# Performance work log

Hardware: AMD Instinct MI355X
Metric: run time of the kernel (lower is better)

Reference implementation:

```python
import jax, jax.numpy as jnp
import numpy as np

N = 100000
IN_F, HID, OUT = 256, 128, 64
NNZ = 1600000
EQ = 200000


def setup_inputs() -> dict:
    key = jax.random.key(0)
    ks = jax.random.split(key, 10)
    x = jax.random.normal(ks[0], (N, IN_F), dtype=jnp.float32)
    adj_rows = jnp.sort(jax.random.randint(ks[1], (NNZ,), 0, N, dtype=jnp.int32))
    adj_cols = jax.random.randint(ks[2], (NNZ,), 0, N, dtype=jnp.int32)
    adj_vals = jax.random.uniform(ks[3], (NNZ,), dtype=jnp.float32)
    edge_index = jax.random.randint(ks[4], (2, EQ), 0, N, dtype=jnp.int32)
    # params (torch Linear default init: U(-1/sqrt(fan_in), 1/sqrt(fan_in)))
    s1 = 1.0 / np.sqrt(IN_F)
    W1 = jax.random.uniform(ks[5], (IN_F, HID), minval=-s1, maxval=s1, dtype=jnp.float32)
    b1 = jax.random.uniform(ks[6], (HID,), minval=-s1, maxval=s1, dtype=jnp.float32)
    s2 = 1.0 / np.sqrt(HID)
    W2 = jax.random.uniform(ks[7], (HID, OUT), minval=-s2, maxval=s2, dtype=jnp.float32)
    b2 = jax.random.uniform(ks[8], (OUT,), minval=-s2, maxval=s2, dtype=jnp.float32)
    return {"x": x, "adj_rows": adj_rows, "adj_cols": adj_cols, "adj_vals": adj_vals,
            "edge_index": edge_index, "W1": W1, "b1": b1, "W2": W2, "b2": b2}


def spmm(rows, cols, vals, dense):
    # out[i,:] = sum_{e: rows[e]==i} vals[e] * dense[cols[e],:]
    msgs = vals[:, None] * dense[cols]  # [nnz, d]
    return jax.ops.segment_sum(msgs, rows, num_segments=N)


def reference(x, adj_rows, adj_cols, adj_vals, edge_index, W1, b1, W2, b2):
    # GCN layer 1: linear then sparse aggregation
    h = spmm(adj_rows, adj_cols, adj_vals, x @ W1 + b1)  # [N, HID]
    h = jax.nn.relu(h)  # dropout is identity in eval mode
    # GCN layer 2
    z = spmm(adj_rows, adj_cols, adj_vals, h @ W2 + b2)  # [N, OUT]
    # decode: gather src/dst embeddings, elementwise dot
    src, dst = edge_index[0], edge_index[1]
    return jnp.sum(z[src] * z[dst], axis=1)  # [EQ]
```

## Files before the change

### kernel.cpp

```cpp
#include <hip/hip_runtime.h>

constexpr int NN    = 100000;
constexpr int NNZ_E = 1600000;
constexpr int EQn   = 200000;
constexpr int INF_  = 256;
constexpr int HIDF  = 128;
constexpr int OUTF  = 64;

typedef float  f32x4  __attribute__((ext_vector_type(4)));
typedef short  bf16x8 __attribute__((ext_vector_type(8)));

__device__ inline unsigned short f2bf(float f) {
    union { float f; unsigned int i; } x; x.f = f;
    unsigned int r = x.i + 0x7fffu + ((x.i >> 16) & 1u);
    return (unsigned short)(r >> 16);
}

__device__ inline void gl2lds16(const void* g, void* l) {
    __builtin_amdgcn_global_load_lds(
        (const __attribute__((address_space(1))) void*)g,
        (__attribute__((address_space(3))) void*)l, 16, 0, 0);
}

__global__ __launch_bounds__(256) void prep(const int* __restrict__ rows,
                                            int* __restrict__ ptr,
                                            const float* __restrict__ W1,
                                            const float* __restrict__ W2,
                                            unsigned short* __restrict__ W1t,
                                            unsigned short* __restrict__ W2t) {
    int i = blockIdx.x * 256 + threadIdx.x;
    if (i <= NN) {
        int lo = 0, hi = NNZ_E;
        while (lo < hi) {
            int mid = (lo + hi) >> 1;
            if (rows[mid] < i) lo = mid + 1; else hi = mid;
        }
        ptr[i] = lo;
    }
    if (i < INF_ * HIDF) {
        int k = i >> 7, n = i & 127;
        W1t[n * INF_ + k] = f2bf(W1[i]);
    }
    if (i < HIDF * OUTF) {
        int k = i >> 6, n = i & 63;
        W2t[n * HIDF + k] = f2bf(W2[i]);
    }
}

template<int K, int NCOLS, int TR, int CGB, bool A_IS_BF16>
__global__ __launch_bounds__(512, 1) void gemm_persist(const void* __restrict__ Av,
                                                       const unsigned short* __restrict__ Bt,
                                                       const float* __restrict__ bias,
                                                       unsigned short* __restrict__ C,
                                                       int M) {
    constexpr int KS   = K / 32;
    constexpr int NT   = 2;
    constexpr int CG   = 1 << CGB;
    constexpr int RB   = 8 / CG;
    static_assert(RB * 16 == TR, "tile rows = 16*RB");
    static_assert(CG * 32 == NCOLS, "cols = 32*CG");
    constexpr int ABPR = A_IS_BF16 ? K * 2 : K * 4;
    constexpr int RPC  = 1024 / ABPR;
    constexpr int NCH  = TR / RPC;
    constexpr int CPWW = NCH / 8;
    constexpr int ABUF = NCH * 1040;
    constexpr int PK   = K + 8;
    constexpr int PADW = NCOLS + 8;
    constexpr int BSB  = NCOLS * PK * 2;
    constexpr int EPB  = TR * PADW * 2;
    static_assert(TR * NCOLS / 8 == 512, "one uint4 store per thread");
    __shared__ __align__(16) unsigned char smem[2 * ABUF + BSB + EPB];
    unsigned char*  Ab = smem;
    unsigned short* Bs = (unsigned short*)(smem + 2 * ABUF);
    unsigned short* ep = (unsigned short*)(smem + 2 * ABUF + BSB);

    const int tid  = threadIdx.x;
    const int wave = tid >> 6;
    const int lane = tid & 63;
    const int quad = lane >> 4;
    const int l16  = lane & 15;
    const int cg   = wave & (CG - 1);
    const int rb   = wave >> CGB;

    for (int i = tid; i < NCOLS * K / 8; i += 512) {
        int n = i / (K / 8), kc = (i % (K / 8)) * 8;
        *(uint4*)&Bs[n * PK + kc] = *(const uint4*)&Bt[(size_t)n * K + kc];
    }

    const int ntiles = (M + TR - 1) / TR;
    const char* abase = (const char*)Av;

    auto stage = [&](int b, int tile0) {
        unsigned char* dst = Ab + b * ABUF;
        #pragma unroll
        for (int j = 0; j < CPWW; ++j) {
            int ch = wave * CPWW + j;
            int r0 = tile0 + ch * RPC;
            if (r0 > M - RPC) r0 = M - RPC;
            gl2lds16(abase + (size_t)r0 * ABPR + lane * 16, dst + ch * 1040);
        }
    };

    int t = blockIdx.x, buf = 0;
    if (t < ntiles) stage(0, t * TR);

    for (; t < ntiles; t += gridDim.x) {
        __syncthreads();
        int tn = t + gridDim.x;
        if (tn < ntiles) stage(1 - buf, tn * TR);

        const unsigned char* ab = Ab + buf * ABUF;
        const int arow = rb * 16 + l16;
        f32x4 acc[NT];
        #pragma unroll
        for (int tt = 0; tt < NT; ++tt) acc[tt] = (f32x4){0.f, 0.f, 0.f, 0.f};

        #pragma unroll
        for (int ks = 0; ks < KS; ++ks) {
            bf16x8 af;
            if constexpr (A_IS_BF16) {
                int flat = arow * ABPR + ks * 64 + quad * 16;
                af = *(const bf16x8*)(ab + (flat >> 10) * 1040 + (flat & 1023));
            } else {
                int flat = arow * ABPR + ks * 128 + quad * 32;
                const unsigned char* p = ab + (flat >> 10) * 1040 + (flat & 1023);
                float4 a0 = *(const float4*)p;
                float4 a1 = *(const float4*)(p + 16);
                af[0] = (short)f2bf(a0.x); af[1] = (short)f2bf(a0.y);
                af[2] = (short)f2bf(a0.z); af[3] = (short)f2bf(a0.w);
                af[4] = (short)f2bf(a1.x); af[5] = (short)f2bf(a1.y);
                af[6] = (short)f2bf(a1.z); af[7] = (short)f2bf(a1.w);
            }
            #pragma unroll
            for (int tt = 0; tt < NT; ++tt) {
                bf16x8 bfr = *(const bf16x8*)&Bs[(cg * 32 + tt * 16 + l16) * PK + ks * 32 + quad * 8];
                acc[tt] = __builtin_amdgcn_mfma_f32_16x16x32_bf16(af, bfr, acc[tt], 0, 0, 0);
            }
        }

        #pragma unroll
        for (int tt = 0; tt < NT; ++tt) {
            const int col = cg * 32 + tt * 16 + l16;
            const float bb = bias[col];
            #pragma unroll
            for (int r = 0; r < 4; ++r)
                ep[(rb * 16 + quad * 4 + r) * PADW + col] = f2bf(acc[tt][r] + bb);
        }
        __syncthreads();
        {
            constexpr int CH = NCOLS / 8;
            int r = tid / CH, cc = tid % CH;
            int grow = t * TR + r;
            if (grow < M)
                *(uint4*)&C[(size_t)grow * NCOLS + cc * 8] =
                    *(const uint4*)&ep[r * PADW + cc * 8];
        }
        buf ^= 1;
    }
}

__device__ inline void fma8_bf16(float* acc, uint4 q, float v) {
    union { unsigned int i; float f; } t;
    #pragma unroll
    for (int p = 0; p < 4; ++p) {
        unsigned int w = (&q.x)[p];
        t.i = w << 16;          acc[2*p]   += v * t.f;
        t.i = w & 0xffff0000u;  acc[2*p+1] += v * t.f;
    }
}

template<int D, bool RELU>
__global__ __launch_bounds__(256) void spmm_bf16(const int* __restrict__ ptr,
                                                 const int* __restrict__ cols,
                                                 const float* __restrict__ vals,
                                                 const unsigned short* __restrict__ dense,
                                                 unsigned short* __restrict__ outm) {
    constexpr int LPR = D / 8;
    constexpr int RPB = 256 / LPR;
    const int lane = threadIdx.x % LPR;
    const int row  = blockIdx.x * RPB + threadIdx.x / LPR;
    if (row >= NN) return;

    int e = ptr[row];
    const int e1 = ptr[row + 1];
    const size_t lo8 = (size_t)lane * 8;
    float acc[8] = {};

    if (e < e1) {
        for (; e + 4 <= e1; e += 4) {
            int   c0 = cols[e],   c1 = cols[e+1], c2 = cols[e+2], c3 = cols[e+3];
            float v0 = vals[e],   v1 = vals[e+1], v2 = vals[e+2], v3 = vals[e+3];
            uint4 q0 = *(const uint4*)&dense[(size_t)c0 * D + lo8];
            uint4 q1 = *(const uint4*)&dense[(size_t)c1 * D + lo8];
            uint4 q2 = *(const uint4*)&dense[(size_t)c2 * D + lo8];
            uint4 q3 = *(const uint4*)&dense[(size_t)c3 * D + lo8];
            fma8_bf16(acc, q0, v0);
            fma8_bf16(acc, q1, v1);
            fma8_bf16(acc, q2, v2);
            fma8_bf16(acc, q3, v3);
        }
        if (e < e1) {
            int i1 = e, i2 = e + 1, i3 = e + 2;
            bool k1 = i1 < e1, k2 = i2 < e1, k3 = i3 < e1;
            i1 = k1 ? i1 : e1 - 1; i2 = k2 ? i2 : e1 - 1; i3 = k3 ? i3 : e1 - 1;
            int   c0 = cols[i1],            c1 = cols[i2],            c2 = cols[i3];
            float v0 = k1 ? vals[i1] : 0.f, v1 = k2 ? vals[i2] : 0.f, v2 = k3 ? vals[i3] : 0.f;
            uint4 q0 = *(const uint4*)&dense[(size_t)c0 * D + lo8];
            uint4 q1 = *(const uint4*)&dense[(size_t)c1 * D + lo8];
            uint4 q2 = *(const uint4*)&dense[(size_t)c2 * D + lo8];
            fma8_bf16(acc, q0, v0);
            fma8_bf16(acc, q1, v1);
            fma8_bf16(acc, q2, v2);
        }
    }

    if (RELU) {
        #pragma unroll
        for (int p = 0; p < 8; ++p) acc[p] = fmaxf(acc[p], 0.f);
    }
    uint4 o;
    #pragma unroll
    for (int p = 0; p < 4; ++p)
        (&o.x)[p] = (unsigned int)f2bf(acc[2*p]) | ((unsigned int)f2bf(acc[2*p+1]) << 16);
    *(uint4*)&outm[(size_t)row * D + lo8] = o;
}

__global__ __launch_bounds__(256) void decode_dot_bf16(const unsigned short* __restrict__ z,
                                                       const int* __restrict__ ei,
                                                       float* __restrict__ outv) {
    constexpr int HALF = EQn / 2;
    const int lane = threadIdx.x & 7;
    const int g    = blockIdx.x * 32 + (threadIdx.x >> 3);
    if (g >= HALF) return;
    const int eA = g, eB = g + HALF;
    const int sA = ei[eA],       dA = ei[EQn + eA];
    const int sB = ei[eB],       dB = ei[EQn + eB];
    uint4 qa0 = *(const uint4*)&z[(size_t)sA * 64 + lane * 8];
    uint4 qb0 = *(const uint4*)&z[(size_t)dA * 64 + lane * 8];
    uint4 qa1 = *(const uint4*)&z[(size_t)sB * 64 + lane * 8];
    uint4 qb1 = *(const uint4*)&z[(size_t)dB * 64 + lane * 8];
    union { unsigned int i; float f; } ta, tb;
    float p0 = 0.f, p1 = 0.f;
    #pragma unroll
    for (int k = 0; k < 4; ++k) {
        unsigned int wa = (&qa0.x)[k], wb = (&qb0.x)[k];
        ta.i = wa << 16;         tb.i = wb << 16;         p0 += ta.f * tb.f;
        ta.i = wa & 0xffff0000u; tb.i = wb & 0xffff0000u; p0 += ta.f * tb.f;
        wa = (&qa1.x)[k]; wb = (&qb1.x)[k];
        ta.i = wa << 16;         tb.i = wb << 16;         p1 += ta.f * tb.f;
        ta.i = wa & 0xffff0000u; tb.i = wb & 0xffff0000u; p1 += ta.f * tb.f;
    }
    p0 += __shfl_xor(p0, 1, 8); p1 += __shfl_xor(p1, 1, 8);
    p0 += __shfl_xor(p0, 2, 8); p1 += __shfl_xor(p1, 2, 8);
    p0 += __shfl_xor(p0, 4, 8); p1 += __shfl_xor(p1, 4, 8);
    if (lane == 0) { outv[eA] = p0; outv[eB] = p1; }
}

extern "C" void kernel_launch(void* const* d_in, const int* in_sizes, int n_in,
                              void* d_out, int out_size, void* d_ws, size_t ws_size,
                              hipStream_t stream) {
    (void)in_sizes; (void)n_in; (void)out_size; (void)ws_size;

    const float* x        = (const float*)d_in[0];
    const int*   adj_rows = (const int*)  d_in[1];
    const int*   adj_cols = (const int*)  d_in[2];
    const float* adj_vals = (const float*)d_in[3];
    const int*   ei       = (const int*)  d_in[4];
    const float* W1       = (const float*)d_in[5];
    const float* b1       = (const float*)d_in[6];
    const float* W2       = (const float*)d_in[7];
    const float* b2       = (const float*)d_in[8];
    float* out = (float*)d_out;

    char* ws = (char*)d_ws;
    int* row_ptr = (int*)ws;
    size_t off = ((size_t)(NN + 1) * sizeof(int) + 511) & ~(size_t)511;
    unsigned short* W1t = (unsigned short*)(ws + off);
    unsigned short* W2t = W1t + (size_t)HIDF * INF_;
    unsigned short* slotA = W2t + (size_t)OUTF * HIDF;
    slotA = (unsigned short*)(((size_t)slotA + 511) & ~(size_t)511);
    unsigned short* slotB = slotA + (size_t)NN * HIDF;

    prep<<<(NN + 256) / 256, 256, 0, stream>>>(adj_rows, row_ptr, W1, W2, W1t, W2t);

    gemm_persist<INF_, HIDF, 32, 2, false><<<256, 512, 0, stream>>>(
        x, W1t, b1, slotA, NN);

    spmm_bf16<HIDF, true><<<(NN + 15) / 16, 256, 0, stream>>>(
        row_ptr, adj_cols, adj_vals, slotA, slotB);

    gemm_persist<HIDF, OUTF, 64, 1, true><<<512, 512, 0, stream>>>(
        slotB, W2t, b2, slotA, NN);

    spmm_bf16<OUTF, false><<<(NN + 31) / 32, 256, 0, stream>>>(
        row_ptr, adj_cols, adj_vals, slotA, slotB);

    decode_dot_bf16<<<(EQn / 2) / 32, 256, 0, stream>>>(slotB, ei, out);
}
```

Before: 293.2 us.

## Map one wavefront per SpMM row with 16-edge batched gathers

Both SpMM kernels now assign a whole 64-lane wavefront to each sparse row instead of a few lanes. Each lane handles 2 bf16 columns (D=128) or 1 column (D=64). Column indices and values are loaded as wave-uniform scalars in batches of 16 edges, which raises memory-level parallelism and removes per-lane index loads. In exchange, each gather is narrower (4 or 2 bytes per lane), and rows with about 16 nonzeros leave many predicated tail iterations.

```diff
diff --git a/kernel.cpp b/kernel.cpp
--- a/kernel.cpp
+++ b/kernel.cpp
@@ -159,70 +159,64 @@
     }
 }
 
-__device__ inline void fma8_bf16(float* acc, uint4 q, float v) {
-    union { unsigned int i; float f; } t;
-    #pragma unroll
-    for (int p = 0; p < 4; ++p) {
-        unsigned int w = (&q.x)[p];
-        t.i = w << 16;          acc[2*p]   += v * t.f;
-        t.i = w & 0xffff0000u;  acc[2*p+1] += v * t.f;
-    }
-}
-
 template<int D, bool RELU>
-__global__ __launch_bounds__(256) void spmm_bf16(const int* __restrict__ ptr,
+__global__ __launch_bounds__(256) void spmm_wave(const int* __restrict__ ptr,
                                                  const int* __restrict__ cols,
                                                  const float* __restrict__ vals,
                                                  const unsigned short* __restrict__ dense,
                                                  unsigned short* __restrict__ outm) {
-    constexpr int LPR = D / 8;
-    constexpr int RPB = 256 / LPR;
-    const int lane = threadIdx.x % LPR;
-    const int row  = blockIdx.x * RPB + threadIdx.x / LPR;
+    const int lane = threadIdx.x & 63;
+    int row = __builtin_amdgcn_readfirstlane(blockIdx.x * 4 + (threadIdx.x >> 6));
     if (row >= NN) return;
 
-    int e = ptr[row];
-    const int e1 = ptr[row + 1];
-    const size_t lo8 = (size_t)lane * 8;
-    float acc[8] = {};
-
-    if (e < e1) {
-        for (; e + 4 <= e1; e += 4) {
-            int   c0 = cols[e],   c1 = cols[e+1], c2 = cols[e+2], c3 = cols[e+3];
-            float v0 = vals[e],   v1 = vals[e+1], v2 = vals[e+2], v3 = vals[e+3];
-            uint4 q0 = *(const uint4*)&dense[(size_t)c0 * D + lo8];
-            uint4 q1 = *(const uint4*)&dense[(size_t)c1 * D + lo8];
-            uint4 q2 = *(const uint4*)&dense[(size_t)c2 * D + lo8];
-            uint4 q3 = *(const uint4*)&dense[(size_t)c3 * D + lo8];
-            fma8_bf16(acc, q0, v0);
-            fma8_bf16(acc, q1, v1);
-            fma8_bf16(acc, q2, v2);
-            fma8_bf16(acc, q3, v3);
-        }
-        if (e < e1) {
-            int i1 = e, i2 = e + 1, i3 = e + 2;
-            bool k1 = i1 < e1, k2 = i2 < e1, k3 = i3 < e1;
-            i1 = k1 ? i1 : e1 - 1; i2 = k2 ? i2 : e1 - 1; i3 = k3 ? i3 : e1 - 1;
-            int   c0 = cols[i1],            c1 = cols[i2],            c2 = cols[i3];
-            float v0 = k1 ? vals[i1] : 0.f, v1 = k2 ? vals[i2] : 0.f, v2 = k3 ? vals[i3] : 0.f;
-            uint4 q0 = *(const uint4*)&dense[(size_t)c0 * D + lo8];
-            uint4 q1 = *(const uint4*)&dense[(size_t)c1 * D + lo8];
-            uint4 q2 = *(const uint4*)&dense[(size_t)c2 * D + lo8];
-            fma8_bf16(acc, q0, v0);
-            fma8_bf16(acc, q1, v1);
-            fma8_bf16(acc, q2, v2);
-        }
-    }
-
-    if (RELU) {
-        #pragma unroll
-        for (int p = 0; p < 8; ++p) acc[p] = fmaxf(acc[p], 0.f);
-    }
-    uint4 o;
-    #pragma unroll
-    for (int p = 0; p < 4; ++p)
-        (&o.x)[p] = (unsigned int)f2bf(acc[2*p]) | ((unsigned int)f2bf(acc[2*p+1]) << 16);
-    *(uint4*)&outm[(size_t)row * D + lo8] = o;
+    const int e0 = __builtin_amdgcn_readfirstlane(ptr[row]);
+    const int e1 = __builtin_amdgcn_readfirstlane(ptr[row + 1]);
+
+    float acc0 = 0.f, acc1 = 0.f;
+
+    for (int e = e0; e < e1; e += 16) {
+        int cc[16]; float vv[16];
+        #pragma unroll
+        for (int j = 0; j < 16; ++j) {
+            int idx = e + j;
+            const bool ok = idx < e1;
+            idx = ok ? idx : e1 - 1;
+            cc[j] = cols[idx];
+            vv[j] = ok ? vals[idx] : 0.f;
+        }
+        if constexpr (D == 128) {
+            unsigned int q[16];
+            #pragma unroll
+            for (int j = 0; j < 16; ++j)
+                q[j] = *(const unsigned int*)&dense[(size_t)cc[j] * D + lane * 2];
+            #pragma unroll
+            for (int j = 0; j < 16; ++j) {
+                union { unsigned int i; float f; } t;
+                t.i = q[j] << 16;          acc0 += vv[j] * t.f;
+                t.i = q[j] & 0xffff0000u;  acc1 += vv[j] * t.f;
+            }
+        } else {
+            unsigned int q[16];
+            #pragma unroll
+            for (int j = 0; j < 16; ++j)
+                q[j] = dense[(size_t)cc[j] * D + lane];
+            #pragma unroll
+            for (int j = 0; j < 16; ++j) {
+                union { unsigned int i; float f; } t;
+                t.i = q[j] << 16;
+                acc0 += vv[j] * t.f;
+            }
+        }
+    }
+
+    if (RELU) { acc0 = fmaxf(acc0, 0.f); acc1 = fmaxf(acc1, 0.f); }
+
+    if constexpr (D == 128) {
+        unsigned int o = (unsigned int)f2bf(acc0) | ((unsigned int)f2bf(acc1) << 16);
+        *(unsigned int*)&outm[(size_t)row * D + lane * 2] = o;
+    } else {
+        outm[(size_t)row * D + lane] = f2bf(acc0);
+    }
 }
 
 __global__ __launch_bounds__(256) void decode_dot_bf16(const unsigned short* __restrict__ z,
@@ -286,13 +280,13 @@
     gemm_persist<INF_, HIDF, 32, 2, false><<<256, 512, 0, stream>>>(
         x, W1t, b1, slotA, NN);
 
-    spmm_bf16<HIDF, true><<<(NN + 15) / 16, 256, 0, stream>>>(
+    spmm_wave<HIDF, true><<<(NN + 3) / 4, 256, 0, stream>>>(
         row_ptr, adj_cols, adj_vals, slotA, slotB);
 
     gemm_persist<HIDF, OUTF, 64, 1, true><<<512, 512, 0, stream>>>(
         slotB, W2t, b2, slotA, NN);
 
-    spmm_bf16<OUTF, false><<<(NN + 31) / 32, 256, 0, stream>>>(
+    spmm_wave<OUTF, false><<<(NN + 3) / 4, 256, 0, stream>>>(
         row_ptr, adj_cols, adj_vals, slotA, slotB);
 
     decode_dot_bf16<<<(EQn / 2) / 32, 256, 0, stream>>>(slotB, ei, out);
```

Measured after the change: 351.9 us. 20.0% more time.

## Pack and sort CSR edges per row, use grid-stride SpMM

Applied to the files above, without the earlier changes.

A new kernel packs each row's column index and value into interleaved int2 records. For rows with up to 64 entries it also bitonic-sorts them by column within a wavefront, so gathers from the dense matrix touch addresses in order. Both SpMM launches read the packed records and use a fixed 2048-block grid-stride loop instead of one block per row group. This adds a launch and an extra pass over the edge arrays in exchange for fewer separate index and value loads and possibly better gather locality.

```diff
diff --git a/kernel.cpp b/kernel.cpp
--- a/kernel.cpp
+++ b/kernel.cpp
@@ -44,6 +44,43 @@
     if (i < HIDF * OUTF) {
         int k = i >> 6, n = i & 63;
         W2t[n * HIDF + k] = f2bf(W2[i]);
+    }
+}
+
+__global__ __launch_bounds__(256) void sort_pack(const int* __restrict__ ptr,
+                                                 const int* __restrict__ cols,
+                                                 const float* __restrict__ vals,
+                                                 int2* __restrict__ ep) {
+    const int lane = threadIdx.x & 63;
+    const int row  = blockIdx.x * 4 + (threadIdx.x >> 6);
+    if (row >= NN) return;
+    const int e0 = ptr[row], e1 = ptr[row + 1];
+    const int n  = e1 - e0;
+    if (n <= 0) return;
+    if (n <= 64) {
+        int key; float v;
+        if (lane < n) { key = (cols[e0 + lane] << 6) | lane; v = vals[e0 + lane]; }
+        else          { key = 0x7fffff00 | lane;             v = 0.f; }
+        #pragma unroll
+        for (int k = 2; k <= 64; k <<= 1) {
+            #pragma unroll
+            for (int j = k >> 1; j > 0; j >>= 1) {
+                int   pk_ = __shfl_xor(key, j, 64);
+                float pv_ = __shfl_xor(v,   j, 64);
+                const bool up    = ((lane & k) == 0);
+                const bool lower = ((lane & j) == 0);
+                if ((key > pk_) == (lower == up)) { key = pk_; v = pv_; }
+            }
+        }
+        if (lane < n) {
+            int2 o; o.x = key >> 6; o.y = __float_as_int(v);
+            ep[e0 + lane] = o;
+        }
+    } else {
+        for (int i = lane; i < n; i += 64) {
+            int2 o; o.x = cols[e0 + i]; o.y = __float_as_int(vals[e0 + i]);
+            ep[e0 + i] = o;
+        }
     }
 }
 
@@ -170,59 +207,64 @@
 }
 
 template<int D, bool RELU>
-__global__ __launch_bounds__(256) void spmm_bf16(const int* __restrict__ ptr,
-                                                 const int* __restrict__ cols,
-                                                 const float* __restrict__ vals,
-                                                 const unsigned short* __restrict__ dense,
-                                                 unsigned short* __restrict__ outm) {
+__global__ __launch_bounds__(256) void spmm_sw(const int* __restrict__ ptr,
+                                               const int2* __restrict__ ep,
+                                               const unsigned short* __restrict__ dense,
+                                               unsigned short* __restrict__ outm) {
     constexpr int LPR = D / 8;
     constexpr int RPB = 256 / LPR;
+    constexpr int NRG = (NN + RPB - 1) / RPB;
     const int lane = threadIdx.x % LPR;
-    const int row  = blockIdx.x * RPB + threadIdx.x / LPR;
-    if (row >= NN) return;
-
-    int e = ptr[row];
-    const int e1 = ptr[row + 1];
+    const int rl   = threadIdx.x / LPR;
     const size_t lo8 = (size_t)lane * 8;
-    float acc[8] = {};
-
-    if (e < e1) {
-        for (; e + 4 <= e1; e += 4) {
-            int   c0 = cols[e],   c1 = cols[e+1], c2 = cols[e+2], c3 = cols[e+3];
-            float v0 = vals[e],   v1 = vals[e+1], v2 = vals[e+2], v3 = vals[e+3];
-            uint4 q0 = *(const uint4*)&dense[(size_t)c0 * D + lo8];
-            uint4 q1 = *(const uint4*)&dense[(size_t)c1 * D + lo8];
-            uint4 q2 = *(const uint4*)&dense[(size_t)c2 * D + lo8];
-            uint4 q3 = *(const uint4*)&dense[(size_t)c3 * D + lo8];
-            fma8_bf16(acc, q0, v0);
-            fma8_bf16(acc, q1, v1);
-            fma8_bf16(acc, q2, v2);
-            fma8_bf16(acc, q3, v3);
-        }
+
+    for (int rg = blockIdx.x; rg < NRG; rg += gridDim.x) {
+        const int row = rg * RPB + rl;
+        if (row >= NN) continue;
+
+        int e = ptr[row];
+        const int e1 = ptr[row + 1];
+        float acc[8] = {};
+
         if (e < e1) {
-            int i1 = e, i2 = e + 1, i3 = e + 2;
-            bool k1 = i1 < e1, k2 = i2 < e1, k3 = i3 < e1;
-            i1 = k1 ? i1 : e1 - 1; i2 = k2 ? i2 : e1 - 1; i3 = k3 ? i3 : e1 - 1;
-            int   c0 = cols[i1],            c1 = cols[i2],            c2 = cols[i3];
-            float v0 = k1 ? vals[i1] : 0.f, v1 = k2 ? vals[i2] : 0.f, v2 = k3 ? vals[i3] : 0.f;
-            uint4 q0 = *(const uint4*)&dense[(size_t)c0 * D + lo8];
-            uint4 q1 = *(const uint4*)&dense[(size_t)c1 * D + lo8];
-            uint4 q2 = *(const uint4*)&dense[(size_t)c2 * D + lo8];
-            fma8_bf16(acc, q0, v0);
-            fma8_bf16(acc, q1, v1);
-            fma8_bf16(acc, q2, v2);
-        }
-    }
-
-    if (RELU) {
-        #pragma unroll
-        for (int p = 0; p < 8; ++p) acc[p] = fmaxf(acc[p], 0.f);
-    }
-    uint4 o;
-    #pragma unroll
-    for (int p = 0; p < 4; ++p)
-        (&o.x)[p] = (unsigned int)f2bf(acc[2*p]) | ((unsigned int)f2bf(acc[2*p+1]) << 16);
-    *(uint4*)&outm[(size_t)row * D + lo8] = o;
+            for (; e + 4 <= e1; e += 4) {
+                int2 p0 = ep[e], p1 = ep[e+1], p2 = ep[e+2], p3 = ep[e+3];
+                uint4 q0 = *(const uint4*)&dense[(size_t)p0.x * D + lo8];
+                uint4 q1 = *(const uint4*)&dense[(size_t)p1.x * D + lo8];
+                uint4 q2 = *(const uint4*)&dense[(size_t)p2.x * D + lo8];
+                uint4 q3 = *(const uint4*)&dense[(size_t)p3.x * D + lo8];
+                fma8_bf16(acc, q0, __int_as_float(p0.y));
+                fma8_bf16(acc, q1, __int_as_float(p1.y));
+                fma8_bf16(acc, q2, __int_as_float(p2.y));
+                fma8_bf16(acc, q3, __int_as_float(p3.y));
+            }
+            if (e < e1) {
+                int i1 = e, i2 = e + 1, i3 = e + 2;
+                bool k1 = i1 < e1, k2 = i2 < e1, k3 = i3 < e1;
+                i1 = k1 ? i1 : e1 - 1; i2 = k2 ? i2 : e1 - 1; i3 = k3 ? i3 : e1 - 1;
+                int2 p0 = ep[i1], p1 = ep[i2], p2 = ep[i3];
+                float v0 = k1 ? __int_as_float(p0.y) : 0.f;
+                float v1 = k2 ? __int_as_float(p1.y) : 0.f;
+                float v2 = k3 ? __int_as_float(p2.y) : 0.f;
+                uint4 q0 = *(const uint4*)&dense[(size_t)p0.x * D + lo8];
+                uint4 q1 = *(const uint4*)&dense[(size_t)p1.x * D + lo8];
+                uint4 q2 = *(const uint4*)&dense[(size_t)p2.x * D + lo8];
+                fma8_bf16(acc, q0, v0);
+                fma8_bf16(acc, q1, v1);
+                fma8_bf16(acc, q2, v2);
+            }
+        }
+
+        if (RELU) {
+            #pragma unroll
+            for (int p = 0; p < 8; ++p) acc[p] = fmaxf(acc[p], 0.f);
+        }
+        uint4 o;
+        #pragma unroll
+        for (int p = 0; p < 4; ++p)
+            (&o.x)[p] = (unsigned int)f2bf(acc[2*p]) | ((unsigned int)f2bf(acc[2*p+1]) << 16);
+        *(uint4*)&outm[(size_t)row * D + lo8] = o;
+    }
 }
 
 __global__ __launch_bounds__(256) void decode_dot_bf16(const unsigned short* __restrict__ z,
@@ -280,20 +322,23 @@
     unsigned short* slotA = W2t + (size_t)OUTF * HIDF;
     slotA = (unsigned short*)(((size_t)slotA + 511) & ~(size_t)511);
     unsigned short* slotB = slotA + (size_t)NN * HIDF;
+    int2* epk = (int2*)(((size_t)(slotB + (size_t)NN * HIDF) + 511) & ~(size_t)511);
 
     prep<<<(NN + 256) / 256, 256, 0, stream>>>(adj_rows, row_ptr, W1, W2, W1t, W2t);
+
+    sort_pack<<<(NN + 3) / 4, 256, 0, stream>>>(row_ptr, adj_cols, adj_vals, epk);
 
     gemm_persist<INF_, HIDF, 32, 2, false><<<256, 512, 0, stream>>>(
         x, W1t, b1, slotA, NN);
 
-    spmm_bf16<HIDF, true><<<(NN + 15) / 16, 256, 0, stream>>>(
-        row_ptr, adj_cols, adj_vals, slotA, slotB);
+    spmm_sw<HIDF, true><<<2048, 256, 0, stream>>>(
+        row_ptr, epk, slotA, slotB);
 
     gemm_persist<HIDF, OUTF, 64, 1, true><<<512, 512, 0, stream>>>(
         slotB, W2t, b2, slotA, NN);
 
-    spmm_bf16<OUTF, false><<<(NN + 31) / 32, 256, 0, stream>>>(
-        row_ptr, adj_cols, adj_vals, slotA, slotB);
+    spmm_sw<OUTF, false><<<2048, 256, 0, stream>>>(
+        row_ptr, epk, slotA, slotB);
 
     decode_dot_bf16<<<(EQn / 2) / 32, 256, 0, stream>>>(slotB, ei, out);
 }
```

After: 338.0 us. 15.3% more time.

## Fuse layer-1 SpMM with ReLU and second linear layer via MFMA epilogue

Applied to the files above, without the earlier changes.

The first sparse aggregation kernel now applies ReLU, stages its 16-row bf16 tile in LDS, and multiplies it by W2 (loaded into LDS per block) with MFMA, adding the bias before writing the 64-wide result. This removes the separate second GEMM launch and the global write and read of the 100000x128 hidden matrix. The cost is that every block reloads the 16KB W2 tile and uses more LDS, which may lower occupancy for the latency-bound gather. The shared accumulation loop is factored into a helper, and the workspace buffers are swapped to match.

```diff
diff --git a/kernel.cpp b/kernel.cpp
--- a/kernel.cpp
+++ b/kernel.cpp
@@ -169,6 +169,103 @@
     }
 }
 
+template<int D>
+__device__ inline void spmm_row_accum(int e, int e1,
+                                      const int* __restrict__ cols,
+                                      const float* __restrict__ vals,
+                                      const unsigned short* __restrict__ dense,
+                                      size_t lo8, float* acc) {
+    if (e >= e1) return;
+    for (; e + 4 <= e1; e += 4) {
+        int   c0 = cols[e],   c1 = cols[e+1], c2 = cols[e+2], c3 = cols[e+3];
+        float v0 = vals[e],   v1 = vals[e+1], v2 = vals[e+2], v3 = vals[e+3];
+        uint4 q0 = *(const uint4*)&dense[(size_t)c0 * D + lo8];
+        uint4 q1 = *(const uint4*)&dense[(size_t)c1 * D + lo8];
+        uint4 q2 = *(const uint4*)&dense[(size_t)c2 * D + lo8];
+        uint4 q3 = *(const uint4*)&dense[(size_t)c3 * D + lo8];
+        fma8_bf16(acc, q0, v0);
+        fma8_bf16(acc, q1, v1);
+        fma8_bf16(acc, q2, v2);
+        fma8_bf16(acc, q3, v3);
+    }
+    if (e < e1) {
+        int i1 = e, i2 = e + 1, i3 = e + 2;
+        bool k1 = i1 < e1, k2 = i2 < e1, k3 = i3 < e1;
+        i1 = k1 ? i1 : e1 - 1; i2 = k2 ? i2 : e1 - 1; i3 = k3 ? i3 : e1 - 1;
+        int   c0 = cols[i1],            c1 = cols[i2],            c2 = cols[i3];
+        float v0 = k1 ? vals[i1] : 0.f, v1 = k2 ? vals[i2] : 0.f, v2 = k3 ? vals[i3] : 0.f;
+        uint4 q0 = *(const uint4*)&dense[(size_t)c0 * D + lo8];
+        uint4 q1 = *(const uint4*)&dense[(size_t)c1 * D + lo8];
+        uint4 q2 = *(const uint4*)&dense[(size_t)c2 * D + lo8];
+        fma8_bf16(acc, q0, v0);
+        fma8_bf16(acc, q1, v1);
+        fma8_bf16(acc, q2, v2);
+    }
+}
+
+__global__ __launch_bounds__(256) void spmm1_fused(const int* __restrict__ ptr,
+                                                   const int* __restrict__ cols,
+                                                   const float* __restrict__ vals,
+                                                   const unsigned short* __restrict__ dense,
+                                                   const unsigned short* __restrict__ W2t,
+                                                   const float* __restrict__ b2,
+                                                   unsigned short* __restrict__ z0) {
+    constexpr int D = 128;
+    static_assert(NN % 16 == 0, "exact tiling, no tail guard");
+    __shared__ __align__(16) unsigned short W2s[64 * 136];
+    __shared__ __align__(16) unsigned short ht[16 * 136];
+    __shared__ __align__(16) unsigned short zt[16 * 72];
+
+    const int tid = threadIdx.x;
+
+    #pragma unroll
+    for (int i = 0; i < 4; ++i) {
+        int idx = tid + i * 256;
+        int r = idx >> 4, ch = idx & 15;
+        *(uint4*)&W2s[r * 136 + ch * 8] = *(const uint4*)&W2t[r * 128 + ch * 8];
+    }
+
+    const int lane16 = tid & 15;
+    const int rl     = tid >> 4;
+    const int row    = blockIdx.x * 16 + rl;
+    const size_t lo8 = (size_t)lane16 * 8;
+    float acc[8] = {};
+    spmm_row_accum<D>(ptr[row], ptr[row + 1], cols, vals, dense, lo8, acc);
+
+    uint4 o;
+    #pragma unroll
+    for (int p = 0; p < 4; ++p) {
+        float a0 = fmaxf(acc[2*p],   0.f);
+        float a1 = fmaxf(acc[2*p+1], 0.f);
+        (&o.x)[p] = (unsigned int)f2bf(a0) | ((unsigned int)f2bf(a1) << 16);
+    }
+    *(uint4*)&ht[rl * 136 + lane16 * 8] = o;
+    __syncthreads();
+
+    const int wv   = tid >> 6;
+    const int lane = tid & 63;
+    const int l16  = lane & 15;
+    const int quad = lane >> 4;
+    f32x4 c = (f32x4){0.f, 0.f, 0.f, 0.f};
+    #pragma unroll
+    for (int ks = 0; ks < 4; ++ks) {
+        bf16x8 af = *(const bf16x8*)&ht[l16 * 136 + ks * 32 + quad * 8];
+        bf16x8 bf_ = *(const bf16x8*)&W2s[(wv * 16 + l16) * 136 + ks * 32 + quad * 8];
+        c = __builtin_amdgcn_mfma_f32_16x16x32_bf16(af, bf_, c, 0, 0, 0);
+    }
+    const float bb = b2[wv * 16 + l16];
+    #pragma unroll
+    for (int r = 0; r < 4; ++r)
+        zt[(quad * 4 + r) * 72 + wv * 16 + l16] = f2bf(c[r] + bb);
+    __syncthreads();
+
+    if (tid < 128) {
+        int r = tid >> 3, cc = tid & 7;
+        *(uint4*)&z0[((size_t)blockIdx.x * 16 + r) * 64 + cc * 8] =
+            *(const uint4*)&zt[r * 72 + cc * 8];
+    }
+}
+
 template<int D, bool RELU>
 __global__ __launch_bounds__(256) void spmm_bf16(const int* __restrict__ ptr,
                                                  const int* __restrict__ cols,
@@ -181,38 +278,9 @@
     const int row  = blockIdx.x * RPB + threadIdx.x / LPR;
     if (row >= NN) return;
 
-    int e = ptr[row];
-    const int e1 = ptr[row + 1];
     const size_t lo8 = (size_t)lane * 8;
     float acc[8] = {};
-
-    if (e < e1) {
-        for (; e + 4 <= e1; e += 4) {
-            int   c0 = cols[e],   c1 = cols[e+1], c2 = cols[e+2], c3 = cols[e+3];
-            float v0 = vals[e],   v1 = vals[e+1], v2 = vals[e+2], v3 = vals[e+3];
-            uint4 q0 = *(const uint4*)&dense[(size_t)c0 * D + lo8];
-            uint4 q1 = *(const uint4*)&dense[(size_t)c1 * D + lo8];
-            uint4 q2 = *(const uint4*)&dense[(size_t)c2 * D + lo8];
-            uint4 q3 = *(const uint4*)&dense[(size_t)c3 * D + lo8];
-            fma8_bf16(acc, q0, v0);
-            fma8_bf16(acc, q1, v1);
-            fma8_bf16(acc, q2, v2);
-            fma8_bf16(acc, q3, v3);
-        }
-        if (e < e1) {
-            int i1 = e, i2 = e + 1, i3 = e + 2;
-            bool k1 = i1 < e1, k2 = i2 < e1, k3 = i3 < e1;
-            i1 = k1 ? i1 : e1 - 1; i2 = k2 ? i2 : e1 - 1; i3 = k3 ? i3 : e1 - 1;
-            int   c0 = cols[i1],            c1 = cols[i2],            c2 = cols[i3];
-            float v0 = k1 ? vals[i1] : 0.f, v1 = k2 ? vals[i2] : 0.f, v2 = k3 ? vals[i3] : 0.f;
-            uint4 q0 = *(const uint4*)&dense[(size_t)c0 * D + lo8];
-            uint4 q1 = *(const uint4*)&dense[(size_t)c1 * D + lo8];
-            uint4 q2 = *(const uint4*)&dense[(size_t)c2 * D + lo8];
-            fma8_bf16(acc, q0, v0);
-            fma8_bf16(acc, q1, v1);
-            fma8_bf16(acc, q2, v2);
-        }
-    }
+    spmm_row_accum<D>(ptr[row], ptr[row + 1], cols, vals, dense, lo8, acc);
 
     if (RELU) {
         #pragma unroll
@@ -286,14 +354,11 @@
     gemm_persist<INF_, HIDF, 32, 2, false><<<256, 512, 0, stream>>>(
         x, W1t, b1, slotA, NN);
 
-    spmm_bf16<HIDF, true><<<(NN + 15) / 16, 256, 0, stream>>>(
-        row_ptr, adj_cols, adj_vals, slotA, slotB);
-
-    gemm_persist<HIDF, OUTF, 64, 1, true><<<512, 512, 0, stream>>>(
-        slotB, W2t, b2, slotA, NN);
+    spmm1_fused<<<NN / 16, 256, 0, stream>>>(
+        row_ptr, adj_cols, adj_vals, slotA, W2t, b2, slotB);
 
     spmm_bf16<OUTF, false><<<(NN + 31) / 32, 256, 0, stream>>>(
-        row_ptr, adj_cols, adj_vals, slotA, slotB);
-
-    decode_dot_bf16<<<(EQn / 2) / 32, 256, 0, stream>>>(slotB, ei, out);
-}
+        row_ptr, adj_cols, adj_vals, slotB, slotA);
+
+    decode_dot_bf16<<<(EQn / 2) / 32, 256, 0, stream>>>(slotA, ei, out);
+}
```

After: 285.7 us. 2.6% less time.
